# Kernel tuning notes

Hardware: AMD Instinct MI355X
Metric: run time of the kernel (lower is better)

Reference implementation:

```python
import jax, jax.numpy as jnp
import numpy as np

EPS = 0.1   # module __init__ default eps
TAU = 1.0   # map_em default tau


def _mog_eval(pi, mu, Sigma, data):
    # pi: (B,p), mu/Sigma: (B,p,d), data: (B,N,d)
    d = data.shape[-1]
    inv_S = 1.0 / Sigma
    jll = -0.5 * (
        d * jnp.log(2.0 * jnp.pi)
        + jnp.log(Sigma).sum(-1)[:, None, :]                      # (B,1,p)
        + jnp.einsum('bnd,bpd->bnp', data * data, inv_S)          # Mahalanobis x^2 term
        + (mu * mu * inv_S).sum(-1)[:, None, :]                   # mu^2/Sigma term
        - 2.0 * jnp.einsum('bnd,bpd->bnp', data, mu * inv_S)      # cross term
    ) + jnp.log(pi)[:, None, :]
    mll = jax.nn.logsumexp(jll, axis=-1)          # (B,N)
    cll = jll - mll[..., None]                    # (B,N,p)
    return jll, cll, mll


def _map_m_step(data, weight, m, V, tau):
    # data: (B,N,d), weight: (B,N,p), m/V: (p,d)
    wsum = weight.sum(1)                                  # (B,p)
    wsum_reg = wsum + tau
    wxsum = jnp.einsum('bnp,bnd->bpd', weight, data)
    wxxsum = jnp.einsum('bnp,bnd->bpd', weight, data * data)
    pi = wsum_reg / wsum_reg.sum(1, keepdims=True)
    mu = (wxsum + m[None] * tau) / wsum_reg[..., None]
    Sigma = (wxxsum + (V + m * m)[None] * tau) / wsum_reg[..., None] - mu * mu
    return pi, mu, Sigma


def setup_inputs() -> dict:
    key = jax.random.key(0)
    k1, k2 = jax.random.split(key)
    B, N, d, p = 8, 4096, 1024, 16
    data = jax.random.normal(k1, (B, N, d), dtype=jnp.float32)
    mask = jnp.ones((B, N), dtype=jnp.float32)
    m = 0.1 * jax.random.normal(k2, (p, d), dtype=jnp.float32)
    V_ = jnp.full((p, d), np.log(np.e - 1.0), dtype=jnp.float32)
    return {"data": data, "mask": mask, "m": m, "V_": V_, "num_iters": 3}


def reference(data, mask, m, V_, num_iters):
    B, N, d = data.shape
    p = m.shape[0]
    # prior (DirNIWNet.forward + mode)
    V = EPS * jax.nn.softplus(V_)
    pi = jnp.full((B, p), 1.0 / p, dtype=data.dtype)
    mu = jnp.broadcast_to(m, (B, p, d)).astype(data.dtype)
    Sigma = jnp.broadcast_to(V, (B, p, d)).astype(data.dtype)
    qq = jnp.zeros((B, N, p), dtype=data.dtype)
    for _ in range(num_iters):  # small fixed iteration count (EM)
        _, cll, _ = _mog_eval(pi, mu, Sigma, data)
        qq = jnp.exp(cll) * mask[..., None]
        pi, mu, Sigma = _map_m_step(data, qq, m, V, TAU)
    return pi, mu, Sigma, qq
```

## Files before the change

### kernel.cpp

```cpp
#include <hip/hip_runtime.h>
#include <math.h>

#define BB 8
#define NN 4096
#define DD 1024
#define PP 16

static constexpr float DLOG2PI = 1881.9861160031696f;
static constexpr float EPSC = 0.1f;


__global__ __launch_bounds__(256) void k_init(const float* __restrict__ m,
                                              const float* __restrict__ V_,
                                              float* __restrict__ Wmat,
                                              float* __restrict__ cns)
{
    int j = blockIdx.x, b = blockIdx.y;
    int tid = threadIdx.x;
    __shared__ float red[512];
    int d0 = tid * 4;
    float4 m4 = *(const float4*)(m + j * DD + d0);
    float4 v4 = *(const float4*)(V_ + j * DD + d0);
    float mv[4] = {m4.x, m4.y, m4.z, m4.w};
    float vv[4] = {v4.x, v4.y, v4.z, v4.w};
    float* Wb = Wmat + (size_t)b * (DD * 32);
    float llog = 0.f, lmq = 0.f;
#pragma unroll
    for (int c = 0; c < 4; c++) {
        float V = EPSC * log1pf(expf(vv[c]));
        float inv = 1.0f / V;
        int d = d0 + c;
        Wb[d * 32 + j * 2] = inv;
        Wb[d * 32 + j * 2 + 1] = mv[c] * inv;
        llog += logf(V);
        lmq += mv[c] * mv[c] * inv;
    }
    red[tid] = llog; red[256 + tid] = lmq;
    __syncthreads();
    for (int s = 128; s > 0; s >>= 1) {
        if (tid < s) { red[tid] += red[tid + s]; red[256 + tid] += red[256 + tid + s]; }
        __syncthreads();
    }
    if (tid == 0)
        cns[b * PP + j] = logf(1.0f / 16.0f) - 0.5f * (DLOG2PI + red[0] + red[256]);
}

__global__ __launch_bounds__(256) void k_estep_part(const float* __restrict__ X,
                                                    const float* __restrict__ Wmat,
                                                    float* __restrict__ epart)
{
    int tile = blockIdx.x, ks = blockIdx.y, b = blockIdx.z;
    int n0 = tile * 128, k0 = ks * 256;
    const float* Xb = X + ((size_t)b * NN + n0) * DD + k0;
    const float* Wb = Wmat + (size_t)b * (DD * 32) + (size_t)k0 * 32;
    __shared__ float Asub[128 * 33];
    __shared__ float Wsub[32 * 36];
    int tid = threadIdx.x;
    int tx = tid & 7, ty = tid >> 3;
    float acc1[4][2] = {{0.f,0.f},{0.f,0.f},{0.f,0.f},{0.f,0.f}};
    float acc2[4][2] = {{0.f,0.f},{0.f,0.f},{0.f,0.f},{0.f,0.f}};
    for (int kk = 0; kk < 256; kk += 32) {
        __syncthreads();
#pragma unroll
        for (int i = 0; i < 4; i++) {
            int f = tid + i * 256;
            int row = f >> 3;
            int kq = (f & 7) << 2;
            float4 v = *(const float4*)(Xb + (size_t)row * DD + kk + kq);
            Asub[row * 33 + kq + 0] = v.x;
            Asub[row * 33 + kq + 1] = v.y;
            Asub[row * 33 + kq + 2] = v.z;
            Asub[row * 33 + kq + 3] = v.w;
        }
        {
            int k = tid >> 3, cq = (tid & 7) << 2;
            *(float4*)(Wsub + k * 36 + cq) = *(const float4*)(Wb + (size_t)(kk + k) * 32 + cq);
        }
        __syncthreads();
#pragma unroll 8
        for (int k = 0; k < 32; k++) {
            float4 w = *(const float4*)(Wsub + k * 36 + tx * 4);
            float a0 = Asub[(ty * 4 + 0) * 33 + k];
            float a1 = Asub[(ty * 4 + 1) * 33 + k];
            float a2 = Asub[(ty * 4 + 2) * 33 + k];
            float a3 = Asub[(ty * 4 + 3) * 33 + k];
            float s0 = a0 * a0, s1 = a1 * a1, s2 = a2 * a2, s3 = a3 * a3;
            acc1[0][0] += s0 * w.x; acc2[0][0] += a0 * w.y; acc1[0][1] += s0 * w.z; acc2[0][1] += a0 * w.w;
            acc1[1][0] += s1 * w.x; acc2[1][0] += a1 * w.y; acc1[1][1] += s1 * w.z; acc2[1][1] += a1 * w.w;
            acc1[2][0] += s2 * w.x; acc2[2][0] += a2 * w.y; acc1[2][1] += s2 * w.z; acc2[2][1] += a2 * w.w;
            acc1[3][0] += s3 * w.x; acc2[3][0] += a3 * w.y; acc1[3][1] += s3 * w.z; acc2[3][1] += a3 * w.w;
        }
    }
    float* ep = epart + (((size_t)ks * BB + b) * NN + n0) * PP;
#pragma unroll
    for (int r = 0; r < 4; r++) {
        float2 v = make_float2(-0.5f * acc1[r][0] + acc2[r][0],
                               -0.5f * acc1[r][1] + acc2[r][1]);
        *(float2*)(ep + (ty * 4 + r) * PP + tx * 2) = v;
    }
}

__global__ __launch_bounds__(128) void k_ereduce(const float* __restrict__ epart,
                                                 const float* __restrict__ mask,
                                                 const float* __restrict__ cns,
                                                 float* __restrict__ qq)
{
    int chunk = blockIdx.x, b = blockIdx.y;
    int tid = threadIdx.x;
    int n = chunk * 128 + tid;
    __shared__ float cs[16];
    if (tid < 16) cs[tid] = cns[b * PP + tid];
    __syncthreads();
    float jl[16];
#pragma unroll
    for (int q = 0; q < 4; q++) {
        float4 v = *(const float4*)(epart + ((size_t)b * NN + n) * PP + q * 4);
        jl[q * 4 + 0] = v.x; jl[q * 4 + 1] = v.y; jl[q * 4 + 2] = v.z; jl[q * 4 + 3] = v.w;
    }
#pragma unroll
    for (int ks = 1; ks < 4; ks++) {
#pragma unroll
        for (int q = 0; q < 4; q++) {
            float4 v = *(const float4*)(epart + (((size_t)ks * BB + b) * NN + n) * PP + q * 4);
            jl[q * 4 + 0] += v.x; jl[q * 4 + 1] += v.y; jl[q * 4 + 2] += v.z; jl[q * 4 + 3] += v.w;
        }
    }
    float mx = -3.4e38f;
#pragma unroll
    for (int j = 0; j < 16; j++) { jl[j] += cs[j]; mx = fmaxf(mx, jl[j]); }
    float sum = 0.f;
#pragma unroll
    for (int j = 0; j < 16; j++) { jl[j] = expf(jl[j] - mx); sum += jl[j]; }
    float r = mask[(size_t)b * NN + n] / sum;
    float* qo = qq + ((size_t)b * NN + n) * PP;
#pragma unroll
    for (int q = 0; q < 4; q++)
        *(float4*)(qo + q * 4) = make_float4(jl[q * 4 + 0] * r, jl[q * 4 + 1] * r,
                                             jl[q * 4 + 2] * r, jl[q * 4 + 3] * r);
}

__global__ __launch_bounds__(256) void k_mstep(const float* __restrict__ X,
                                               const float* __restrict__ qq,
                                               float* __restrict__ wxp,
                                               float* __restrict__ wxxp)
{
    int cc = blockIdx.x, nq = blockIdx.y, b = blockIdx.z;
    int tid = threadIdx.x;
    int cg = tid & 15, rg = tid >> 4;
    int col0 = cc * 64 + cg * 4;
    const float* Xb = X + ((size_t)b * NN + nq * 512) * DD;
    const float* qb = qq + ((size_t)b * NN + nq * 512) * PP;
    float aw[16][4] = {};
    float ax[16][4] = {};
    for (int i = 0; i < 32; i++) {
        int n = i * 16 + rg;
        float4 x = *(const float4*)(Xb + (size_t)n * DD + col0);
        const float4 q0 = *(const float4*)(qb + n * PP + 0);
        const float4 q1 = *(const float4*)(qb + n * PP + 4);
        const float4 q2 = *(const float4*)(qb + n * PP + 8);
        const float4 q3 = *(const float4*)(qb + n * PP + 12);
        float x2x = x.x * x.x, x2y = x.y * x.y, x2z = x.z * x.z, x2w = x.w * x.w;
        float qv[16] = {q0.x, q0.y, q0.z, q0.w, q1.x, q1.y, q1.z, q1.w,
                        q2.x, q2.y, q2.z, q2.w, q3.x, q3.y, q3.z, q3.w};
#pragma unroll
        for (int jj = 0; jj < 16; jj++) {
            float qj = qv[jj];
            aw[jj][0] += qj * x.x; aw[jj][1] += qj * x.y; aw[jj][2] += qj * x.z; aw[jj][3] += qj * x.w;
            ax[jj][0] += qj * x2x; ax[jj][1] += qj * x2y; ax[jj][2] += qj * x2z; ax[jj][3] += qj * x2w;
        }
    }
    __shared__ float red[16 * 548];
#pragma unroll
    for (int ph = 0; ph < 4; ph++) {
        int jb = (ph & 1) * 8;
        __syncthreads();
#pragma unroll
        for (int jj = 0; jj < 8; jj++) {
            float4 v;
            if (ph < 2) v = make_float4(aw[jb + jj][0], aw[jb + jj][1], aw[jb + jj][2], aw[jb + jj][3]);
            else        v = make_float4(ax[jb + jj][0], ax[jb + jj][1], ax[jb + jj][2], ax[jb + jj][3]);
            *(float4*)(red + rg * 548 + jj * 68 + cg * 4) = v;
        }
        __syncthreads();
        float* dst = (ph < 2) ? wxp : wxxp;
#pragma unroll
        for (int o = 0; o < 2; o++) {
            int idx = tid + o * 256;
            int jj = idx >> 6, c = idx & 63;
            float s = 0.f;
#pragma unroll
            for (int g = 0; g < 16; g++) s += red[g * 548 + jj * 68 + c];
            dst[(((size_t)b * 8 + nq) * PP + jb + jj) * DD + cc * 64 + c] = s;
        }
    }
}

__global__ __launch_bounds__(256) void k_finalize(const float* __restrict__ qq,
                                                  const float* __restrict__ wxp,
                                                  const float* __restrict__ wxxp,
                                                  const float* __restrict__ m,
                                                  const float* __restrict__ V_,
                                                  float* __restrict__ pi,
                                                  float* __restrict__ mu,
                                                  float* __restrict__ Sigma,
                                                  float* __restrict__ Wmat,
                                                  float* __restrict__ cns)
{
    int j = blockIdx.x, b = blockIdx.y;
    int tid = threadIdx.x;
    __shared__ float red[256 * 17 + 8];
    __shared__ float wsr[16];
    __shared__ float sden;
    const float* qb = qq + (size_t)b * NN * PP;
    float ws[16] = {0,0,0,0,0,0,0,0,0,0,0,0,0,0,0,0};
    for (int i = 0; i < 16; i++) {
        int n = tid + i * 256;
        const float4 q0 = *(const float4*)(qb + (size_t)n * PP + 0);
        const float4 q1 = *(const float4*)(qb + (size_t)n * PP + 4);
        const float4 q2 = *(const float4*)(qb + (size_t)n * PP + 8);
        const float4 q3 = *(const float4*)(qb + (size_t)n * PP + 12);
        ws[0] += q0.x; ws[1] += q0.y; ws[2] += q0.z; ws[3] += q0.w;
        ws[4] += q1.x; ws[5] += q1.y; ws[6] += q1.z; ws[7] += q1.w;
        ws[8] += q2.x; ws[9] += q2.y; ws[10] += q2.z; ws[11] += q2.w;
        ws[12] += q3.x; ws[13] += q3.y; ws[14] += q3.z; ws[15] += q3.w;
    }
#pragma unroll
    for (int jj = 0; jj < 16; jj++) red[tid * 17 + jj] = ws[jj];
    __syncthreads();
    if (tid < 16) {
        float s = 0.f;
        for (int t = 0; t < 256; t++) s += red[t * 17 + tid];
        wsr[tid] = s + 1.0f;
    }
    __syncthreads();
    if (tid == 0) {
        float dd = 0.f;
#pragma unroll
        for (int jj = 0; jj < 16; jj++) dd += wsr[jj];
        sden = dd;
    }
    __syncthreads();
    float rws = 1.0f / wsr[j];
    float pij = wsr[j] / sden;
    int d0 = tid * 4;
    float wxa[4] = {0, 0, 0, 0}, wxxa[4] = {0, 0, 0, 0};
#pragma unroll
    for (int g = 0; g < 8; g++) {
        const float4 a = *(const float4*)(wxp + (((size_t)b * 8 + g) * PP + j) * DD + d0);
        wxa[0] += a.x; wxa[1] += a.y; wxa[2] += a.z; wxa[3] += a.w;
        const float4 c2 = *(const float4*)(wxxp + (((size_t)b * 8 + g) * PP + j) * DD + d0);
        wxxa[0] += c2.x; wxxa[1] += c2.y; wxxa[2] += c2.z; wxxa[3] += c2.w;
    }
    float4 m4 = *(const float4*)(m + j * DD + d0);
    float4 v4 = *(const float4*)(V_ + j * DD + d0);
    float mvv[4] = {m4.x, m4.y, m4.z, m4.w};
    float vvv[4] = {v4.x, v4.y, v4.z, v4.w};
    float muo[4], sgo[4];
    float llog = 0.f, lmq = 0.f;
    float* Wb = Wmat + (size_t)b * (DD * 32);
#pragma unroll
    for (int c = 0; c < 4; c++) {
        float V = EPSC * log1pf(expf(vvv[c]));
        float muv = (wxa[c] + mvv[c]) * rws;
        float Sg = (wxxa[c] + V + mvv[c] * mvv[c]) * rws - muv * muv;
        float inv = 1.0f / Sg;
        muo[c] = muv; sgo[c] = Sg;
        int d = d0 + c;
        Wb[d * 32 + j * 2] = inv;
        Wb[d * 32 + j * 2 + 1] = muv * inv;
        llog += logf(Sg);
        lmq += muv * muv * inv;
    }
    *(float4*)(mu + ((size_t)b * PP + j) * DD + d0) = make_float4(muo[0], muo[1], muo[2], muo[3]);
    *(float4*)(Sigma + ((size_t)b * PP + j) * DD + d0) = make_float4(sgo[0], sgo[1], sgo[2], sgo[3]);
    red[tid] = llog; red[4096 + tid] = lmq;
    __syncthreads();
    for (int s = 128; s > 0; s >>= 1) {
        if (tid < s) { red[tid] += red[tid + s]; red[4096 + tid] += red[4096 + tid + s]; }
        __syncthreads();
    }
    if (tid == 0) {
        pi[b * PP + j] = pij;
        cns[b * PP + j] = logf(pij) - 0.5f * (DLOG2PI + red[0] + red[4096]);
    }
}

extern "C" void kernel_launch(void* const* d_in, const int* in_sizes, int n_in,
                              void* d_out, int out_size, void* d_ws, size_t ws_size,
                              hipStream_t stream)
{
    (void)in_sizes; (void)n_in; (void)out_size; (void)ws_size;
    const float* data = (const float*)d_in[0];
    const float* mask = (const float*)d_in[1];
    const float* m    = (const float*)d_in[2];
    const float* V_   = (const float*)d_in[3];

    float* out = (float*)d_out;
    float* pi  = out;
    float* mu  = out + 128;
    float* Sg  = out + 128 + 131072;
    float* qq  = out + 128 + 2 * 131072;

    float* ws    = (float*)d_ws;
    float* Wmat  = ws;
    float* cns   = ws + 262144;
    float* epart = ws + 262272;
    float* wxp   = ws + 262272 + 2097152;
    float* wxxp  = ws + 262272 + 2097152 + 1048576;

    k_init<<<dim3(16, 8), 256, 0, stream>>>(m, V_, Wmat, cns);
    for (int it = 0; it < 3; it++) {
        k_estep_part<<<dim3(32, 4, 8), 256, 0, stream>>>(data, Wmat, epart);
        k_ereduce<<<dim3(32, 8), 128, 0, stream>>>(epart, mask, cns, qq);
        k_mstep<<<dim3(16, 8, 8), 256, 0, stream>>>(data, qq, wxp, wxxp);
        k_finalize<<<dim3(16, 8), 256, 0, stream>>>(qq, wxp, wxxp, m, V_, pi, mu, Sg, Wmat, cns);
    }
}
```

Before: 468.6 us.

## Fuse E-step GEMM with softmax reduction, drop split-K partial buffer

Merges the split-K E-step partial GEMM and the separate reduce/softmax kernel into one kernel. Each block now covers 64 rows over the full 1024-wide K dimension and applies the logsumexp normalization in shared memory, removing the epart workspace round-trip and one launch per iteration. It also adds register prefetching of the next K-tile to overlap global loads with compute. In exchange the grid shrinks from 1024 blocks to 512, and each block runs a longer serial K loop, which may reduce parallelism on a large GPU.

```diff
diff --git a/kernel.cpp b/kernel.cpp
--- a/kernel.cpp
+++ b/kernel.cpp
@@ -45,98 +45,95 @@
         cns[b * PP + j] = logf(1.0f / 16.0f) - 0.5f * (DLOG2PI + red[0] + red[256]);
 }
 
-__global__ __launch_bounds__(256) void k_estep_part(const float* __restrict__ X,
-                                                    const float* __restrict__ Wmat,
-                                                    float* __restrict__ epart)
-{
-    int tile = blockIdx.x, ks = blockIdx.y, b = blockIdx.z;
-    int n0 = tile * 128, k0 = ks * 256;
-    const float* Xb = X + ((size_t)b * NN + n0) * DD + k0;
-    const float* Wb = Wmat + (size_t)b * (DD * 32) + (size_t)k0 * 32;
-    __shared__ float Asub[128 * 33];
+__global__ __launch_bounds__(256) void k_estep(const float* __restrict__ X,
+                                               const float* __restrict__ Wmat,
+                                               const float* __restrict__ mask,
+                                               const float* __restrict__ cns,
+                                               float* __restrict__ qq)
+{
+    int tile = blockIdx.x, b = blockIdx.y;
+    int n0 = tile * 64;
+    const float* Xb = X + ((size_t)b * NN + n0) * DD;
+    const float* Wb = Wmat + (size_t)b * (DD * 32);
+    __shared__ float Asub[64 * 36];
     __shared__ float Wsub[32 * 36];
+    __shared__ float sjl[64 * 17];
+    __shared__ float cs[16];
     int tid = threadIdx.x;
     int tx = tid & 7, ty = tid >> 3;
-    float acc1[4][2] = {{0.f,0.f},{0.f,0.f},{0.f,0.f},{0.f,0.f}};
-    float acc2[4][2] = {{0.f,0.f},{0.f,0.f},{0.f,0.f},{0.f,0.f}};
-    for (int kk = 0; kk < 256; kk += 32) {
-        __syncthreads();
-#pragma unroll
-        for (int i = 0; i < 4; i++) {
-            int f = tid + i * 256;
-            int row = f >> 3;
-            int kq = (f & 7) << 2;
-            float4 v = *(const float4*)(Xb + (size_t)row * DD + kk + kq);
-            Asub[row * 33 + kq + 0] = v.x;
-            Asub[row * 33 + kq + 1] = v.y;
-            Asub[row * 33 + kq + 2] = v.z;
-            Asub[row * 33 + kq + 3] = v.w;
-        }
-        {
-            int k = tid >> 3, cq = (tid & 7) << 2;
-            *(float4*)(Wsub + k * 36 + cq) = *(const float4*)(Wb + (size_t)(kk + k) * 32 + cq);
-        }
-        __syncthreads();
-#pragma unroll 8
-        for (int k = 0; k < 32; k++) {
-            float4 w = *(const float4*)(Wsub + k * 36 + tx * 4);
-            float a0 = Asub[(ty * 4 + 0) * 33 + k];
-            float a1 = Asub[(ty * 4 + 1) * 33 + k];
-            float a2 = Asub[(ty * 4 + 2) * 33 + k];
-            float a3 = Asub[(ty * 4 + 3) * 33 + k];
-            float s0 = a0 * a0, s1 = a1 * a1, s2 = a2 * a2, s3 = a3 * a3;
-            acc1[0][0] += s0 * w.x; acc2[0][0] += a0 * w.y; acc1[0][1] += s0 * w.z; acc2[0][1] += a0 * w.w;
-            acc1[1][0] += s1 * w.x; acc2[1][0] += a1 * w.y; acc1[1][1] += s1 * w.z; acc2[1][1] += a1 * w.w;
-            acc1[2][0] += s2 * w.x; acc2[2][0] += a2 * w.y; acc1[2][1] += s2 * w.z; acc2[2][1] += a2 * w.w;
-            acc1[3][0] += s3 * w.x; acc2[3][0] += a3 * w.y; acc1[3][1] += s3 * w.z; acc2[3][1] += a3 * w.w;
-        }
-    }
-    float* ep = epart + (((size_t)ks * BB + b) * NN + n0) * PP;
-#pragma unroll
-    for (int r = 0; r < 4; r++) {
-        float2 v = make_float2(-0.5f * acc1[r][0] + acc2[r][0],
-                               -0.5f * acc1[r][1] + acc2[r][1]);
-        *(float2*)(ep + (ty * 4 + r) * PP + tx * 2) = v;
-    }
-}
-
-__global__ __launch_bounds__(128) void k_ereduce(const float* __restrict__ epart,
-                                                 const float* __restrict__ mask,
-                                                 const float* __restrict__ cns,
-                                                 float* __restrict__ qq)
-{
-    int chunk = blockIdx.x, b = blockIdx.y;
-    int tid = threadIdx.x;
-    int n = chunk * 128 + tid;
-    __shared__ float cs[16];
     if (tid < 16) cs[tid] = cns[b * PP + tid];
-    __syncthreads();
-    float jl[16];
-#pragma unroll
-    for (int q = 0; q < 4; q++) {
-        float4 v = *(const float4*)(epart + ((size_t)b * NN + n) * PP + q * 4);
-        jl[q * 4 + 0] = v.x; jl[q * 4 + 1] = v.y; jl[q * 4 + 2] = v.z; jl[q * 4 + 3] = v.w;
-    }
-#pragma unroll
-    for (int ks = 1; ks < 4; ks++) {
-#pragma unroll
-        for (int q = 0; q < 4; q++) {
-            float4 v = *(const float4*)(epart + (((size_t)ks * BB + b) * NN + n) * PP + q * 4);
-            jl[q * 4 + 0] += v.x; jl[q * 4 + 1] += v.y; jl[q * 4 + 2] += v.z; jl[q * 4 + 3] += v.w;
-        }
-    }
-    float mx = -3.4e38f;
-#pragma unroll
-    for (int j = 0; j < 16; j++) { jl[j] += cs[j]; mx = fmaxf(mx, jl[j]); }
-    float sum = 0.f;
-#pragma unroll
-    for (int j = 0; j < 16; j++) { jl[j] = expf(jl[j] - mx); sum += jl[j]; }
-    float r = mask[(size_t)b * NN + n] / sum;
-    float* qo = qq + ((size_t)b * NN + n) * PP;
-#pragma unroll
-    for (int q = 0; q < 4; q++)
-        *(float4*)(qo + q * 4) = make_float4(jl[q * 4 + 0] * r, jl[q * 4 + 1] * r,
-                                             jl[q * 4 + 2] * r, jl[q * 4 + 3] * r);
+
+    int srow = tid >> 3;
+    int skq  = (tid & 7) << 2;
+
+    float4 pa0, pa1, pw;
+    pa0 = *(const float4*)(Xb + (size_t)srow * DD + skq);
+    pa1 = *(const float4*)(Xb + (size_t)(srow + 32) * DD + skq);
+    pw  = *(const float4*)(Wb + (size_t)srow * 32 + skq);
+    *(float4*)(Asub + srow * 36 + skq) = pa0;
+    *(float4*)(Asub + (srow + 32) * 36 + skq) = pa1;
+    *(float4*)(Wsub + srow * 36 + skq) = pw;
+
+    float m1[2][2] = {{0.f,0.f},{0.f,0.f}};
+    float m2[2][2] = {{0.f,0.f},{0.f,0.f}};
+    __syncthreads();
+
+    for (int kk = 0; kk < DD; kk += 32) {
+        if (kk + 32 < DD) {
+            pa0 = *(const float4*)(Xb + (size_t)srow * DD + kk + 32 + skq);
+            pa1 = *(const float4*)(Xb + (size_t)(srow + 32) * DD + kk + 32 + skq);
+            pw  = *(const float4*)(Wb + (size_t)(kk + 32 + srow) * 32 + skq);
+        }
+        float s1[2][2] = {{0.f,0.f},{0.f,0.f}};
+        float s2[2][2] = {{0.f,0.f},{0.f,0.f}};
+#pragma unroll 4
+        for (int k = 0; k < 32; k += 2) {
+            float4 w0 = *(const float4*)(Wsub + k * 36 + tx * 4);
+            float4 w1 = *(const float4*)(Wsub + (k + 1) * 36 + tx * 4);
+            float2 a0 = *(const float2*)(Asub + (2 * ty) * 36 + k);
+            float2 a1 = *(const float2*)(Asub + (2 * ty + 1) * 36 + k);
+            float q0 = a0.x * a0.x, q1 = a1.x * a1.x;
+            s1[0][0] += q0 * w0.x; s2[0][0] += a0.x * w0.y; s1[0][1] += q0 * w0.z; s2[0][1] += a0.x * w0.w;
+            s1[1][0] += q1 * w0.x; s2[1][0] += a1.x * w0.y; s1[1][1] += q1 * w0.z; s2[1][1] += a1.x * w0.w;
+            float q2 = a0.y * a0.y, q3 = a1.y * a1.y;
+            s1[0][0] += q2 * w1.x; s2[0][0] += a0.y * w1.y; s1[0][1] += q2 * w1.z; s2[0][1] += a0.y * w1.w;
+            s1[1][0] += q3 * w1.x; s2[1][0] += a1.y * w1.y; s1[1][1] += q3 * w1.z; s2[1][1] += a1.y * w1.w;
+        }
+#pragma unroll
+        for (int r = 0; r < 2; r++)
+#pragma unroll
+            for (int c = 0; c < 2; c++) { m1[r][c] += s1[r][c]; m2[r][c] += s2[r][c]; }
+        __syncthreads();
+        if (kk + 32 < DD) {
+            *(float4*)(Asub + srow * 36 + skq) = pa0;
+            *(float4*)(Asub + (srow + 32) * 36 + skq) = pa1;
+            *(float4*)(Wsub + srow * 36 + skq) = pw;
+        }
+        __syncthreads();
+    }
+
+#pragma unroll
+    for (int r = 0; r < 2; r++)
+#pragma unroll
+        for (int c = 0; c < 2; c++)
+            sjl[(2 * ty + r) * 17 + 2 * tx + c] = -0.5f * m1[r][c] + m2[r][c];
+    __syncthreads();
+    if (tid < 64) {
+        int n = n0 + tid;
+        float jl[16];
+        float mx = -3.4e38f;
+#pragma unroll
+        for (int j = 0; j < 16; j++) { jl[j] = sjl[tid * 17 + j] + cs[j]; mx = fmaxf(mx, jl[j]); }
+        float sum = 0.f;
+#pragma unroll
+        for (int j = 0; j < 16; j++) { jl[j] = expf(jl[j] - mx); sum += jl[j]; }
+        float r = mask[(size_t)b * NN + n] / sum;
+        float* qo = qq + ((size_t)b * NN + n) * PP;
+#pragma unroll
+        for (int q = 0; q < 4; q++)
+            *(float4*)(qo + q * 4) = make_float4(jl[q * 4 + 0] * r, jl[q * 4 + 1] * r,
+                                                 jl[q * 4 + 2] * r, jl[q * 4 + 3] * r);
+    }
 }
 
 __global__ __launch_bounds__(256) void k_mstep(const float* __restrict__ X,
@@ -304,14 +301,12 @@
     float* ws    = (float*)d_ws;
     float* Wmat  = ws;
     float* cns   = ws + 262144;
-    float* epart = ws + 262272;
-    float* wxp   = ws + 262272 + 2097152;
-    float* wxxp  = ws + 262272 + 2097152 + 1048576;
+    float* wxp   = ws + 262272;
+    float* wxxp  = ws + 262272 + 1048576;
 
     k_init<<<dim3(16, 8), 256, 0, stream>>>(m, V_, Wmat, cns);
     for (int it = 0; it < 3; it++) {
-        k_estep_part<<<dim3(32, 4, 8), 256, 0, stream>>>(data, Wmat, epart);
-        k_ereduce<<<dim3(32, 8), 128, 0, stream>>>(epart, mask, cns, qq);
+        k_estep<<<dim3(64, 8), 256, 0, stream>>>(data, Wmat, mask, cns, qq);
         k_mstep<<<dim3(16, 8, 8), 256, 0, stream>>>(data, qq, wxp, wxxp);
         k_finalize<<<dim3(16, 8), 256, 0, stream>>>(qq, wxp, wxxp, m, V_, pi, mu, Sg, Wmat, cns);
     }
```

New measurement: 487.4 us. 1.04x slower.

## Split M-step components across half-blocks and raise E-step K-split to eight

Applied to the files above, without the earlier changes.

The M-step kernel now gives each half of the block eight of the sixteen mixture components. This halves the per-thread accumulator registers, and a launch bound asks for four blocks per CU, both aimed at higher occupancy. Each thread now covers 64 rows instead of 32, and the shared reduction buffer shrinks. The E-step GEMM splits K into eight parts when the workspace is large enough, which doubles its grid to fill the GPU but makes the reduce kernel read more partial sums.

```diff
diff --git a/kernel.cpp b/kernel.cpp
--- a/kernel.cpp
+++ b/kernel.cpp
@@ -47,10 +47,11 @@
 
 __global__ __launch_bounds__(256) void k_estep_part(const float* __restrict__ X,
                                                     const float* __restrict__ Wmat,
-                                                    float* __restrict__ epart)
+                                                    float* __restrict__ epart,
+                                                    int klen)
 {
     int tile = blockIdx.x, ks = blockIdx.y, b = blockIdx.z;
-    int n0 = tile * 128, k0 = ks * 256;
+    int n0 = tile * 128, k0 = ks * klen;
     const float* Xb = X + ((size_t)b * NN + n0) * DD + k0;
     const float* Wb = Wmat + (size_t)b * (DD * 32) + (size_t)k0 * 32;
     __shared__ float Asub[128 * 33];
@@ -59,7 +60,7 @@
     int tx = tid & 7, ty = tid >> 3;
     float acc1[4][2] = {{0.f,0.f},{0.f,0.f},{0.f,0.f},{0.f,0.f}};
     float acc2[4][2] = {{0.f,0.f},{0.f,0.f},{0.f,0.f},{0.f,0.f}};
-    for (int kk = 0; kk < 256; kk += 32) {
+    for (int kk = 0; kk < klen; kk += 32) {
         __syncthreads();
 #pragma unroll
         for (int i = 0; i < 4; i++) {
@@ -103,7 +104,8 @@
 __global__ __launch_bounds__(128) void k_ereduce(const float* __restrict__ epart,
                                                  const float* __restrict__ mask,
                                                  const float* __restrict__ cns,
-                                                 float* __restrict__ qq)
+                                                 float* __restrict__ qq,
+                                                 int nparts)
 {
     int chunk = blockIdx.x, b = blockIdx.y;
     int tid = threadIdx.x;
@@ -117,8 +119,7 @@
         float4 v = *(const float4*)(epart + ((size_t)b * NN + n) * PP + q * 4);
         jl[q * 4 + 0] = v.x; jl[q * 4 + 1] = v.y; jl[q * 4 + 2] = v.z; jl[q * 4 + 3] = v.w;
     }
-#pragma unroll
-    for (int ks = 1; ks < 4; ks++) {
+    for (int ks = 1; ks < nparts; ks++) {
 #pragma unroll
         for (int q = 0; q < 4; q++) {
             float4 v = *(const float4*)(epart + (((size_t)ks * BB + b) * NN + n) * PP + q * 4);
@@ -139,47 +140,48 @@
                                              jl[q * 4 + 2] * r, jl[q * 4 + 3] * r);
 }
 
-__global__ __launch_bounds__(256) void k_mstep(const float* __restrict__ X,
-                                               const float* __restrict__ qq,
-                                               float* __restrict__ wxp,
-                                               float* __restrict__ wxxp)
+__global__ __launch_bounds__(256, 4) void k_mstep(const float* __restrict__ X,
+                                                  const float* __restrict__ qq,
+                                                  float* __restrict__ wxp,
+                                                  float* __restrict__ wxxp)
 {
     int cc = blockIdx.x, nq = blockIdx.y, b = blockIdx.z;
     int tid = threadIdx.x;
-    int cg = tid & 15, rg = tid >> 4;
+    int cg = tid & 15;
+    int rg = (tid >> 4) & 7;
+    int jh = tid >> 7;
     int col0 = cc * 64 + cg * 4;
     const float* Xb = X + ((size_t)b * NN + nq * 512) * DD;
     const float* qb = qq + ((size_t)b * NN + nq * 512) * PP;
-    float aw[16][4] = {};
-    float ax[16][4] = {};
-    for (int i = 0; i < 32; i++) {
-        int n = i * 16 + rg;
+    float aw[8][4] = {};
+    float ax[8][4] = {};
+    for (int i = 0; i < 64; i++) {
+        int n = i * 8 + rg;
         float4 x = *(const float4*)(Xb + (size_t)n * DD + col0);
-        const float4 q0 = *(const float4*)(qb + n * PP + 0);
-        const float4 q1 = *(const float4*)(qb + n * PP + 4);
-        const float4 q2 = *(const float4*)(qb + n * PP + 8);
-        const float4 q3 = *(const float4*)(qb + n * PP + 12);
+        const float4 q0 = *(const float4*)(qb + n * PP + jh * 8);
+        const float4 q1 = *(const float4*)(qb + n * PP + jh * 8 + 4);
         float x2x = x.x * x.x, x2y = x.y * x.y, x2z = x.z * x.z, x2w = x.w * x.w;
-        float qv[16] = {q0.x, q0.y, q0.z, q0.w, q1.x, q1.y, q1.z, q1.w,
-                        q2.x, q2.y, q2.z, q2.w, q3.x, q3.y, q3.z, q3.w};
-#pragma unroll
-        for (int jj = 0; jj < 16; jj++) {
+        float qv[8] = {q0.x, q0.y, q0.z, q0.w, q1.x, q1.y, q1.z, q1.w};
+#pragma unroll
+        for (int jj = 0; jj < 8; jj++) {
             float qj = qv[jj];
             aw[jj][0] += qj * x.x; aw[jj][1] += qj * x.y; aw[jj][2] += qj * x.z; aw[jj][3] += qj * x.w;
             ax[jj][0] += qj * x2x; ax[jj][1] += qj * x2y; ax[jj][2] += qj * x2z; ax[jj][3] += qj * x2w;
         }
     }
-    __shared__ float red[16 * 548];
+    __shared__ float red[8 * 548];
 #pragma unroll
     for (int ph = 0; ph < 4; ph++) {
         int jb = (ph & 1) * 8;
         __syncthreads();
-#pragma unroll
-        for (int jj = 0; jj < 8; jj++) {
-            float4 v;
-            if (ph < 2) v = make_float4(aw[jb + jj][0], aw[jb + jj][1], aw[jb + jj][2], aw[jb + jj][3]);
-            else        v = make_float4(ax[jb + jj][0], ax[jb + jj][1], ax[jb + jj][2], ax[jb + jj][3]);
-            *(float4*)(red + rg * 548 + jj * 68 + cg * 4) = v;
+        if (jh == (ph & 1)) {
+#pragma unroll
+            for (int jj = 0; jj < 8; jj++) {
+                float4 v;
+                if (ph < 2) v = make_float4(aw[jj][0], aw[jj][1], aw[jj][2], aw[jj][3]);
+                else        v = make_float4(ax[jj][0], ax[jj][1], ax[jj][2], ax[jj][3]);
+                *(float4*)(red + rg * 548 + jj * 68 + cg * 4) = v;
+            }
         }
         __syncthreads();
         float* dst = (ph < 2) ? wxp : wxxp;
@@ -189,7 +191,7 @@
             int jj = idx >> 6, c = idx & 63;
             float s = 0.f;
 #pragma unroll
-            for (int g = 0; g < 16; g++) s += red[g * 548 + jj * 68 + c];
+            for (int g = 0; g < 8; g++) s += red[g * 548 + jj * 68 + c];
             dst[(((size_t)b * 8 + nq) * PP + jb + jj) * DD + cc * 64 + c] = s;
         }
     }
@@ -289,7 +291,7 @@
                               void* d_out, int out_size, void* d_ws, size_t ws_size,
                               hipStream_t stream)
 {
-    (void)in_sizes; (void)n_in; (void)out_size; (void)ws_size;
+    (void)in_sizes; (void)n_in; (void)out_size;
     const float* data = (const float*)d_in[0];
     const float* mask = (const float*)d_in[1];
     const float* m    = (const float*)d_in[2];
@@ -301,17 +303,22 @@
     float* Sg  = out + 128 + 131072;
     float* qq  = out + 128 + 2 * 131072;
 
+    size_t need8 = ((size_t)262272 + (size_t)8 * BB * NN * PP
+                    + (size_t)2 * BB * 8 * PP * DD) * sizeof(float);
+    int KS = (ws_size >= need8) ? 8 : 4;
+    int klen = DD / KS;
+
     float* ws    = (float*)d_ws;
     float* Wmat  = ws;
     float* cns   = ws + 262144;
     float* epart = ws + 262272;
-    float* wxp   = ws + 262272 + 2097152;
-    float* wxxp  = ws + 262272 + 2097152 + 1048576;
+    float* wxp   = epart + (size_t)KS * BB * NN * PP;
+    float* wxxp  = wxp + (size_t)BB * 8 * PP * DD;
 
     k_init<<<dim3(16, 8), 256, 0, stream>>>(m, V_, Wmat, cns);
     for (int it = 0; it < 3; it++) {
-        k_estep_part<<<dim3(32, 4, 8), 256, 0, stream>>>(data, Wmat, epart);
-        k_ereduce<<<dim3(32, 8), 128, 0, stream>>>(epart, mask, cns, qq);
+        k_estep_part<<<dim3(32, KS, 8), 256, 0, stream>>>(data, Wmat, epart, klen);
+        k_ereduce<<<dim3(32, 8), 128, 0, stream>>>(epart, mask, cns, qq, KS);
         k_mstep<<<dim3(16, 8, 8), 256, 0, stream>>>(data, qq, wxp, wxxp);
         k_finalize<<<dim3(16, 8), 256, 0, stream>>>(qq, wxp, wxxp, m, V_, pi, mu, Sg, Wmat, cns);
     }
```

Measured after the change: 459.8 us. Within noise of the previous version (-1.9%).
